# Kernel optimization log

Hardware: AMD Instinct MI355X
Metric: run time of the kernel (lower is better)

The kernel has to match this reference:

```python
import jax, jax.numpy as jnp
import numpy as np

N_TOK, BATCH, D, MEM, H, W = 196, 64, 256, 2048, 16, 16


def setup_inputs() -> dict:
    key = jax.random.key(0)
    ks = jax.random.split(key, 9)
    w_scale = 1.0 / np.sqrt(D)  # ~ Linear default init scale
    return {
        "input_tokens": jax.random.normal(ks[0], (N_TOK, BATCH, D), jnp.float32),
        "ch_memory": jax.random.normal(ks[1], (MEM, D), jnp.float32) * 0.1,
        "ch_wq": jax.random.normal(ks[2], (D, D), jnp.float32) * w_scale,
        "ch_wk": jax.random.normal(ks[3], (D, D), jnp.float32) * w_scale,
        "ch_wv": jax.random.normal(ks[4], (D, D), jnp.float32) * w_scale,
        "sp_memory": jax.random.normal(ks[5], (MEM, H, W), jnp.float32) * 0.1,
        "sp_wq": jax.random.normal(ks[6], (D, D), jnp.float32) * w_scale,
        "sp_wk": jax.random.normal(ks[7], (D, D), jnp.float32) * w_scale,
        "sp_wv": jax.random.normal(ks[8], (D, D), jnp.float32) * w_scale,
    }


def reference(input_tokens, ch_memory, ch_wq, ch_wk, ch_wv,
              sp_memory, sp_wq, sp_wk, sp_wv):
    n_tok, batch, d = input_tokens.shape
    hw = d  # spatial branch requires feature_dim == H*W
    x = input_tokens.reshape(n_tok * batch, d)  # [NB, D]

    # ---- Channel memory branch: dot-product softmax read ----
    q = x @ ch_wq.T                       # [NB, D]
    k = ch_memory @ ch_wk.T               # [M, D]
    v = ch_memory @ ch_wv.T               # [M, D]
    scores = (q @ k.T) * (1.0 / jnp.sqrt(jnp.float32(d)))  # [NB, M]
    att_c = jax.nn.softmax(scores, axis=-1)
    out_c = att_c @ v                     # [NB, D]

    # ---- Spatial memory branch: SSIM-score softmax read ----
    mem_flat = sp_memory.reshape(sp_memory.shape[0], hw)  # [M, HW]
    qf = x @ sp_wq.T                      # [NB, HW]
    kf = mem_flat @ sp_wk.T               # [M, HW]
    vf = mem_flat @ sp_wv.T               # [M, HW]

    q_mean = jnp.mean(qf, axis=1, keepdims=True)          # [NB, 1]
    k_mean = jnp.mean(kf, axis=1, keepdims=True)          # [M, 1]
    q_var = jnp.var(qf, axis=1, ddof=1, keepdims=True)    # unbiased, like torch.var
    k_var = jnp.var(kf, axis=1, ddof=1, keepdims=True)
    cov = ((qf - q_mean) @ (kf - k_mean).T) / jnp.float32(hw - 1)  # [NB, M]

    c1, c2 = 0.01, 0.03
    mean_prod = q_mean @ k_mean.T                          # [NB, M]
    numerator = (2.0 * mean_prod + c1) * (2.0 * cov + c2)
    denominator = (q_mean ** 2 + (k_mean.T) ** 2 + c1) * (q_var + k_var.T + c2)
    ssim = numerator / (denominator + 1e-8)                # [NB, M]

    att_s = jax.nn.softmax(ssim, axis=-1)
    out_s = att_s @ vf                     # [NB, HW] == [NB, D]

    return (out_c + out_s).reshape(n_tok, batch, d)
```

## Files before the change

### kernel.cpp

```cpp
#include <hip/hip_runtime.h>

#define NBQ 12544
#define DM  256
#define MM  2048

typedef __attribute__((ext_vector_type(8)))  __bf16 bf16x8;
typedef __attribute__((ext_vector_type(4)))  float  floatx4;

__device__ __forceinline__ ushort f2bf(float x) {
    unsigned u = __float_as_uint(x);
    u += 0x7fffu + ((u >> 16) & 1u);
    return (ushort)(u >> 16);
}
__device__ __forceinline__ float bf2f(ushort h) {
    return __uint_as_float(((unsigned)h) << 16);
}
__device__ __forceinline__ ushort4 cvt4(float4 f) {
    union { __bf16 h[4]; ushort4 u; } r;
    r.h[0] = (__bf16)f.x; r.h[1] = (__bf16)f.y;
    r.h[2] = (__bf16)f.z; r.h[3] = (__bf16)f.w;
    return r.u;
}

__device__ __forceinline__ void glds16(const ushort* g, ushort* l) {
    __builtin_amdgcn_global_load_lds(
        (const __attribute__((address_space(1))) unsigned int*)g,
        (__attribute__((address_space(3))) unsigned int*)l, 16, 0, 0);
}

#define WAITVM(N) asm volatile("s_waitcnt vmcnt(" #N ")" ::: "memory")
#define WAITLGKM0 asm volatile("s_waitcnt lgkmcnt(0)" ::: "memory")

__global__ __launch_bounds__(256) void gemm_proj_all(
    const float* __restrict__ x,      const float* __restrict__ ch_mem,
    const float* __restrict__ ch_wq,  const float* __restrict__ ch_wk,
    const float* __restrict__ ch_wv,  const float* __restrict__ sp_mem,
    const float* __restrict__ sp_wq,  const float* __restrict__ sp_wk,
    const float* __restrict__ sp_wv,
    ushort* __restrict__ Qb,  ushort* __restrict__ QFb,
    ushort* __restrict__ Kb,  ushort* __restrict__ KFb,
    ushort* __restrict__ Vtb, ushort* __restrict__ VFtb)
{
    __shared__ ushort As[64][72];
    __shared__ ushort W1s[64][72];
    __shared__ ushort W2s[64][72];

    int bid = blockIdx.x;
    const float* A; const float* W1; const float* W2;
    ushort* C1; ushort* C2; int nrows, trans2;
    if (bid < 784) {
        A = x; W1 = ch_wq; W2 = sp_wq; C1 = Qb; C2 = QFb; nrows = NBQ; trans2 = 0;
    } else if (bid < 912) {
        A = ch_mem; W1 = ch_wk; W2 = ch_wv; C1 = Kb; C2 = Vtb;
        nrows = MM; trans2 = 1; bid -= 784;
    } else {
        A = sp_mem; W1 = sp_wk; W2 = sp_wv; C1 = KFb; C2 = VFtb;
        nrows = MM; trans2 = 1; bid -= 912;
    }
    const int r0 = (bid >> 2) * 64;
    const int c0 = (bid & 3) * 64;

    const int tid  = threadIdx.x;
    const int wv   = tid >> 6;
    const int lane = tid & 63;
    const int quad = lane >> 4;
    const int l16  = lane & 15;
    const int rw = (wv & 1) * 32;
    const int cw = (wv >> 1) * 32;

    floatx4 acc1[2][2], acc2[2][2];
    #pragma unroll
    for (int i = 0; i < 2; ++i)
        #pragma unroll
        for (int j = 0; j < 2; ++j) {
            acc1[i][j] = (floatx4){0.f, 0.f, 0.f, 0.f};
            acc2[i][j] = (floatx4){0.f, 0.f, 0.f, 0.f};
        }

    float4 a4[4], w14[4], w24[4];
    #pragma unroll
    for (int it = 0; it < 4; ++it) {
        int idx = tid + it * 256;
        int r = idx >> 4, c4 = (idx & 15) * 4;
        a4[it]  = *(const float4*)(A  + (size_t)(r0 + r) * 256 + c4);
        w14[it] = *(const float4*)(W1 + (size_t)(c0 + r) * 256 + c4);
        w24[it] = *(const float4*)(W2 + (size_t)(c0 + r) * 256 + c4);
    }

    for (int d0 = 0; d0 < 256; d0 += 64) {
        __syncthreads();
        #pragma unroll
        for (int it = 0; it < 4; ++it) {
            int idx = tid + it * 256;
            int r = idx >> 4, c4 = (idx & 15) * 4;
            *(ushort4*)&As[r][c4]  = cvt4(a4[it]);
            *(ushort4*)&W1s[r][c4] = cvt4(w14[it]);
            *(ushort4*)&W2s[r][c4] = cvt4(w24[it]);
        }
        if (d0 + 64 < 256) {
            #pragma unroll
            for (int it = 0; it < 4; ++it) {
                int idx = tid + it * 256;
                int r = idx >> 4, c4 = (idx & 15) * 4;
                a4[it]  = *(const float4*)(A  + (size_t)(r0 + r) * 256 + d0 + 64 + c4);
                w14[it] = *(const float4*)(W1 + (size_t)(c0 + r) * 256 + d0 + 64 + c4);
                w24[it] = *(const float4*)(W2 + (size_t)(c0 + r) * 256 + d0 + 64 + c4);
            }
        }
        __syncthreads();
        #pragma unroll
        for (int kk = 0; kk < 64; kk += 32) {
            bf16x8 aA0 = *(const bf16x8*)&As[rw + l16][kk + quad * 8];
            bf16x8 aA1 = *(const bf16x8*)&As[rw + 16 + l16][kk + quad * 8];
            bf16x8 b10 = *(const bf16x8*)&W1s[cw + l16][kk + quad * 8];
            bf16x8 b11 = *(const bf16x8*)&W1s[cw + 16 + l16][kk + quad * 8];
            bf16x8 b20 = *(const bf16x8*)&W2s[cw + l16][kk + quad * 8];
            bf16x8 b21 = *(const bf16x8*)&W2s[cw + 16 + l16][kk + quad * 8];
            acc1[0][0] = __builtin_amdgcn_mfma_f32_16x16x32_bf16(aA0, b10, acc1[0][0], 0, 0, 0);
            acc1[0][1] = __builtin_amdgcn_mfma_f32_16x16x32_bf16(aA0, b11, acc1[0][1], 0, 0, 0);
            acc1[1][0] = __builtin_amdgcn_mfma_f32_16x16x32_bf16(aA1, b10, acc1[1][0], 0, 0, 0);
            acc1[1][1] = __builtin_amdgcn_mfma_f32_16x16x32_bf16(aA1, b11, acc1[1][1], 0, 0, 0);
            acc2[0][0] = __builtin_amdgcn_mfma_f32_16x16x32_bf16(aA0, b20, acc2[0][0], 0, 0, 0);
            acc2[0][1] = __builtin_amdgcn_mfma_f32_16x16x32_bf16(aA0, b21, acc2[0][1], 0, 0, 0);
            acc2[1][0] = __builtin_amdgcn_mfma_f32_16x16x32_bf16(aA1, b20, acc2[1][0], 0, 0, 0);
            acc2[1][1] = __builtin_amdgcn_mfma_f32_16x16x32_bf16(aA1, b21, acc2[1][1], 0, 0, 0);
        }
    }

    #pragma unroll
    for (int ag = 0; ag < 2; ++ag)
        #pragma unroll
        for (int cg = 0; cg < 2; ++cg)
            #pragma unroll
            for (int i = 0; i < 4; ++i)
                C1[(size_t)(r0 + rw + ag * 16 + quad * 4 + i) * 256
                   + c0 + cw + cg * 16 + l16] = f2bf(acc1[ag][cg][i]);

    if (!trans2) {
        #pragma unroll
        for (int ag = 0; ag < 2; ++ag)
            #pragma unroll
            for (int cg = 0; cg < 2; ++cg)
                #pragma unroll
                for (int i = 0; i < 4; ++i)
                    C2[(size_t)(r0 + rw + ag * 16 + quad * 4 + i) * 256
                       + c0 + cw + cg * 16 + l16] = f2bf(acc2[ag][cg][i]);
    } else {
        __syncthreads();
        #pragma unroll
        for (int ag = 0; ag < 2; ++ag)
            #pragma unroll
            for (int cg = 0; cg < 2; ++cg)
                #pragma unroll
                for (int i = 0; i < 4; ++i)
                    W2s[cw + cg * 16 + l16][rw + ag * 16 + quad * 4 + i] = f2bf(acc2[ag][cg][i]);
        __syncthreads();
        const int col = tid >> 2;
        const int seg = (tid & 3) * 16;
        #pragma unroll
        for (int j = 0; j < 2; ++j)
            *(uint4*)(C2 + (size_t)(c0 + col) * nrows + r0 + seg + j * 8) =
                *(const uint4*)&W2s[col][seg + j * 8];
    }
}

__global__ __launch_bounds__(256) void row_stats_kf(
    const ushort* __restrict__ KFb, float* __restrict__ km, float* __restrict__ kv)
{
    const int row  = blockIdx.x * 4 + (threadIdx.x >> 6);
    const int lane = threadIdx.x & 63;
    ushort4 u = *(const ushort4*)(KFb + (size_t)row * 256 + lane * 4);
    float a = bf2f(u.x), b = bf2f(u.y), c = bf2f(u.z), d = bf2f(u.w);
    float s  = a + b + c + d;
    float ss = a * a + b * b + c * c + d * d;
    #pragma unroll
    for (int off = 32; off > 0; off >>= 1) {
        s  += __shfl_down(s, off);
        ss += __shfl_down(ss, off);
    }
    if (lane == 0) {
        float m = s * (1.f / 256.f);
        km[row] = m;
        kv[row] = (ss - 256.f * m * m) * (1.f / 255.f) + 0.03f;
    }
}

#define STAGE_TILE(b, ti)                                                     \
    {                                                                         \
        const ushort* kp_ = kp0 + (size_t)(ti) * 32 * DM;                     \
        const ushort* vp_ = vp0 + (ti) * 32;                                  \
        ushort* dst_ = SMu + (b) * 16384;                                     \
        _Pragma("unroll")                                                     \
        for (int p = 0; p < 4; ++p) {                                         \
            int db = (wv * 4 + p) * 512;                                      \
            glds16(kp_ + offK[p], dst_ + db);                                 \
            glds16(vp_ + offV[p], dst_ + 8192 + db);                          \
        }                                                                     \
    }

__global__ __launch_bounds__(256, 2) void fused_attn_x4(
    const ushort* __restrict__ Qb,  const ushort* __restrict__ QFb,
    const ushort* __restrict__ Kb,  const ushort* __restrict__ KFb,
    const ushort* __restrict__ Vtb, const ushort* __restrict__ VFtb,
    const float* __restrict__ km_, const float* __restrict__ kv_,
    float* __restrict__ part, float* __restrict__ denp)
{
    __shared__ ushort SMu[32768];

    const int tid  = threadIdx.x;
    const int wv   = tid >> 6;
    const int lane = tid & 63;
    const int quad = lane >> 4;
    const int l16  = lane & 15;

    const int k8   = blockIdx.x & 7;
    const int j    = blockIdx.x >> 3;
    const int br   = (j >= 49) ? 1 : 0;
    const int half = k8 & 3;
    const int qc   = (k8 >> 2) * 49 + (br ? j - 49 : j);
    const int q0   = qc * 128;
    const int kbase = half * 512;
    const int NT   = 16;

    const ushort* qsrc = br ? QFb : Qb;
    const ushort* Ksel = br ? KFb : Kb;
    const ushort* Vsel = br ? VFtb : Vtb;

    bf16x8 aQ0[8], aQ1[8];
    {
        const ushort* qp = qsrc + (size_t)(q0 + wv * 32 + l16) * DM + quad * 8;
        #pragma unroll
        for (int s = 0; s < 8; ++s) {
            aQ0[s] = __builtin_nontemporal_load((const bf16x8*)(qp + s * 32));
            aQ1[s] = __builtin_nontemporal_load((const bf16x8*)(qp + 16 * DM + s * 32));
        }
    }

    float qmv0 = 0.f, qvv0 = 0.f, qmv1 = 0.f, qvv1 = 0.f, qm2_0 = 0.f, qm2_1 = 0.f;
    if (br) {
        float s0 = 0.f, ss0 = 0.f, s1 = 0.f, ss1 = 0.f;
        #pragma unroll
        for (int s = 0; s < 8; ++s)
            #pragma unroll
            for (int jj = 0; jj < 8; ++jj) {
                float v0 = (float)aQ0[s][jj], v1 = (float)aQ1[s][jj];
                s0 += v0; ss0 += v0 * v0; s1 += v1; ss1 += v1 * v1;
            }
        s0  += __shfl_xor(s0, 16, 64);  s0  += __shfl_xor(s0, 32, 64);
        ss0 += __shfl_xor(ss0, 16, 64); ss0 += __shfl_xor(ss0, 32, 64);
        s1  += __shfl_xor(s1, 16, 64);  s1  += __shfl_xor(s1, 32, 64);
        ss1 += __shfl_xor(ss1, 16, 64); ss1 += __shfl_xor(ss1, 32, 64);
        qmv0 = s0 * (1.f / 256.f);
        qvv0 = (ss0 - 256.f * qmv0 * qmv0) * (1.f / 255.f);
        qmv1 = s1 * (1.f / 256.f);
        qvv1 = (ss1 - 256.f * qmv1 * qmv1) * (1.f / 255.f);
        qm2_0 = qmv0 * qmv0 + 0.01f;
        qm2_1 = qmv1 * qmv1 + 0.01f;
    }

    int offK[4], offV[4];
    #pragma unroll
    for (int p = 0; p < 4; ++p) {
        int jw = wv * 4 + p;
        int Rk = 2 * jw + (lane >> 5);
        int rk = (Rk & 3) + ((Rk >> 4) & 1) * 4 + ((Rk >> 2) & 3) * 8;
        int ck = (lane & 31) ^ (Rk & 7);
        offK[p] = rk * DM + ck * 8;
        int Rv = 16 * jw + (lane >> 2);
        int cv = (lane & 3) ^ (Rv & 3);
        offV[p] = Rv * MM + cv * 8;
    }

    const ushort* kp0 = Ksel + (size_t)kbase * DM;
    const ushort* vp0 = Vsel + kbase;

    floatx4 acc0[16], acc1[16];
    #pragma unroll
    for (int t = 0; t < 16; ++t) {
        acc0[t] = (floatx4){0.f, 0.f, 0.f, 0.f};
        acc1[t] = (floatx4){0.f, 0.f, 0.f, 0.f};
    }
    float den0 = 0.f, den1 = 0.f;
    const int ksw  = l16 & 7;
    const int vswo = (quad ^ (l16 & 3)) * 8;

    floatx4 kmc0 = {0,0,0,0}, kmc1 = {0,0,0,0}, kvc0 = {0,0,0,0}, kvc1 = {0,0,0,0};

    STAGE_TILE(0, 0);
    if (br) {
        kmc0 = *(const floatx4*)(km_ + kbase + 8 * quad);
        kmc1 = *(const floatx4*)(km_ + kbase + 8 * quad + 4);
        kvc0 = *(const floatx4*)(kv_ + kbase + 8 * quad);
        kvc1 = *(const floatx4*)(kv_ + kbase + 8 * quad + 4);
    }

    int buf = 0;
    for (int ti = 0; ti < NT; ++ti) {
        const bool have_next = (ti + 1 < NT);
        floatx4 kmn0 = {0,0,0,0}, kmn1 = {0,0,0,0}, kvn0 = {0,0,0,0}, kvn1 = {0,0,0,0};
        if (have_next) {
            STAGE_TILE(buf ^ 1, ti + 1);
            if (br) {
                const int kk1 = kbase + (ti + 1) * 32;
                kmn0 = *(const floatx4*)(km_ + kk1 + 8 * quad);
                kmn1 = *(const floatx4*)(km_ + kk1 + 8 * quad + 4);
                kvn0 = *(const floatx4*)(kv_ + kk1 + 8 * quad);
                kvn1 = *(const floatx4*)(kv_ + kk1 + 8 * quad + 4);
            }
        }
        if (have_next) { if (br) WAITVM(12); else WAITVM(8); }
        else           { WAITVM(0); }
        __builtin_amdgcn_sched_barrier(0);
        __builtin_amdgcn_s_barrier();
        __builtin_amdgcn_sched_barrier(0);

        const ushort* Ks = SMu + buf * 16384;
        const ushort* Vs = Ks + 8192;

        floatx4 S00 = (floatx4){0.f, 0.f, 0.f, 0.f};
        floatx4 S10 = (floatx4){0.f, 0.f, 0.f, 0.f};
        floatx4 S01 = (floatx4){0.f, 0.f, 0.f, 0.f};
        floatx4 S11 = (floatx4){0.f, 0.f, 0.f, 0.f};
        #pragma unroll
        for (int s = 0; s < 8; ++s) {
            int off = ((s * 4 + quad) ^ ksw) * 8;
            bf16x8 aK0 = *(const bf16x8*)(Ks + l16 * DM + off);
            bf16x8 aK1 = *(const bf16x8*)(Ks + 4096 + l16 * DM + off);
            S00 = __builtin_amdgcn_mfma_f32_16x16x32_bf16(aK0, aQ0[s], S00, 0, 0, 0);
            S10 = __builtin_amdgcn_mfma_f32_16x16x32_bf16(aK1, aQ0[s], S10, 0, 0, 0);
            S01 = __builtin_amdgcn_mfma_f32_16x16x32_bf16(aK0, aQ1[s], S01, 0, 0, 0);
            S11 = __builtin_amdgcn_mfma_f32_16x16x32_bf16(aK1, aQ1[s], S11, 0, 0, 0);
        }

        float p0[8], p1[8];
        if (!br) {
            #pragma unroll
            for (int r = 0; r < 4; ++r) {
                p0[r]     = __expf(S00[r] * 0.0625f);
                p0[4 + r] = __expf(S10[r] * 0.0625f);
                p1[r]     = __expf(S01[r] * 0.0625f);
                p1[4 + r] = __expf(S11[r] * 0.0625f);
            }
        } else {
            #pragma unroll
            for (int r = 0; r < 4; ++r) {
                {
                    float kmr = kmc0[r];
                    float mp  = qmv0 * kmr;
                    float cov = (S00[r] - 256.f * mp) * (1.f / 255.f);
                    float num = (2.f * mp + 0.01f) * (2.f * cov + 0.03f);
                    float dn  = (qm2_0 + kmr * kmr) * (qvv0 + kvc0[r]) + 1e-8f;
                    p0[r] = __expf(num / dn);
                }
                {
                    float kmr = kmc1[r];
                    float mp  = qmv0 * kmr;
                    float cov = (S10[r] - 256.f * mp) * (1.f / 255.f);
                    float num = (2.f * mp + 0.01f) * (2.f * cov + 0.03f);
                    float dn  = (qm2_0 + kmr * kmr) * (qvv0 + kvc1[r]) + 1e-8f;
                    p0[4 + r] = __expf(num / dn);
                }
                {
                    float kmr = kmc0[r];
                    float mp  = qmv1 * kmr;
                    float cov = (S01[r] - 256.f * mp) * (1.f / 255.f);
                    float num = (2.f * mp + 0.01f) * (2.f * cov + 0.03f);
                    float dn  = (qm2_1 + kmr * kmr) * (qvv1 + kvc0[r]) + 1e-8f;
                    p1[r] = __expf(num / dn);
                }
                {
                    float kmr = kmc1[r];
                    float mp  = qmv1 * kmr;
                    float cov = (S11[r] - 256.f * mp) * (1.f / 255.f);
                    float num = (2.f * mp + 0.01f) * (2.f * cov + 0.03f);
                    float dn  = (qm2_1 + kmr * kmr) * (qvv1 + kvc1[r]) + 1e-8f;
                    p1[4 + r] = __expf(num / dn);
                }
            }
        }
        union { __bf16 h[8]; bf16x8 v; } ap0, ap1;
        #pragma unroll
        for (int jj = 0; jj < 8; ++jj) {
            den0 += p0[jj]; ap0.h[jj] = (__bf16)p0[jj];
            den1 += p1[jj]; ap1.h[jj] = (__bf16)p1[jj];
        }

        #pragma unroll
        for (int t = 0; t < 16; ++t) {
            bf16x8 bV = *(const bf16x8*)(Vs + (t * 16 + l16) * 32 + vswo);
            acc0[t] = __builtin_amdgcn_mfma_f32_16x16x32_bf16(ap0.v, bV, acc0[t], 0, 0, 0);
            acc1[t] = __builtin_amdgcn_mfma_f32_16x16x32_bf16(ap1.v, bV, acc1[t], 0, 0, 0);
        }

        WAITLGKM0;
        __builtin_amdgcn_sched_barrier(0);
        __builtin_amdgcn_s_barrier();
        __builtin_amdgcn_sched_barrier(0);

        kmc0 = kmn0; kmc1 = kmn1; kvc0 = kvn0; kvc1 = kvn1;
        buf ^= 1;
    }

    den0 += __shfl_xor(den0, 16, 64); den0 += __shfl_xor(den0, 32, 64);
    den1 += __shfl_xor(den1, 16, 64); den1 += __shfl_xor(den1, 32, 64);

    const int sec = br * 4 + half;
    float* Np = part + (size_t)sec * ((size_t)NBQ * DM);
    #pragma unroll
    for (int t = 0; t < 16; ++t)
        #pragma unroll
        for (int r = 0; r < 4; ++r) {
            int row = q0 + wv * 32 + quad * 4 + r;
            __builtin_nontemporal_store(acc0[t][r], &Np[(size_t)row * DM + t * 16 + l16]);
            __builtin_nontemporal_store(acc1[t][r], &Np[(size_t)(row + 16) * DM + t * 16 + l16]);
        }
    if (lane < 16) {
        denp[(size_t)sec * NBQ + q0 + wv * 32 + lane]      = den0;
        denp[(size_t)sec * NBQ + q0 + wv * 32 + 16 + lane] = den1;
    }
}

__global__ __launch_bounds__(256, 2) void fused_attn_fb(
    const ushort* __restrict__ Qb,  const ushort* __restrict__ QFb,
    const ushort* __restrict__ Kb,  const ushort* __restrict__ KFb,
    const ushort* __restrict__ Vtb, const ushort* __restrict__ VFtb,
    const float* __restrict__ km_, const float* __restrict__ kv_,
    float* __restrict__ out)
{
    __shared__ ushort SMu[32768];
    float* combuf = (float*)SMu;

    const int tid  = threadIdx.x;
    const int wv   = tid >> 6;
    const int lane = tid & 63;
    const int quad = lane >> 4;
    const int l16  = lane & 15;
    const int qsel = wv & 1;
    const int br   = wv >> 1;
    const int q0   = blockIdx.x * 32;

    const ushort* qsrc = br ? QFb : Qb;
    bf16x8 aQ[8];
    {
        const ushort* qp = qsrc + (size_t)(q0 + qsel * 16 + l16) * DM + quad * 8;
        #pragma unroll
        for (int s = 0; s < 8; ++s) aQ[s] = *(const bf16x8*)(qp + s * 32);
    }

    float qmv = 0.f, qvv = 0.f, qm2 = 0.f;
    if (br) {
        float sum = 0.f, ss = 0.f;
        #pragma unroll
        for (int s = 0; s < 8; ++s)
            #pragma unroll
            for (int jj = 0; jj < 8; ++jj) {
                float v = (float)aQ[s][jj];
                sum += v; ss += v * v;
            }
        sum += __shfl_xor(sum, 16, 64); sum += __shfl_xor(sum, 32, 64);
        ss  += __shfl_xor(ss, 16, 64);  ss  += __shfl_xor(ss, 32, 64);
        qmv = sum * (1.f / 256.f);
        qvv = (ss - 256.f * qmv * qmv) * (1.f / 255.f);
        qm2 = qmv * qmv + 0.01f;
    }

    int offK[4], offV[4];
    #pragma unroll
    for (int p = 0; p < 4; ++p) {
        int jw = wv * 4 + p;
        int Rk = 2 * jw + (lane >> 5);
        int rk = (Rk & 3) + ((Rk >> 4) & 1) * 4 + ((Rk >> 2) & 3) * 8;
        int ck = (lane & 31) ^ (Rk & 7);
        offK[p] = rk * DM + ck * 8;
        int Rv = 16 * jw + (lane >> 2);
        int cv = (lane & 3) ^ (Rv & 3);
        offV[p] = Rv * MM + cv * 8;
    }

    const ushort* kp  = Kb;
    const ushort* kfp = KFb;
    const ushort* vp  = Vtb;
    const ushort* vfp = VFtb;

    floatx4 acc[16];
    #pragma unroll
    for (int t = 0; t < 16; ++t) acc[t] = (floatx4){0.f, 0.f, 0.f, 0.f};
    float den = 0.f;

    const int ksw  = l16 & 7;
    const int vswo = (quad ^ (l16 & 3)) * 8;

    for (int kt = 0; kt < MM; kt += 32) {
        __syncthreads();
        #pragma unroll
        for (int p = 0; p < 4; ++p) {
            int db = (wv * 4 + p) * 512;
            glds16(kp  + offK[p], SMu + db);
            glds16(kfp + offK[p], SMu + 8192 + db);
            glds16(vp  + offV[p], SMu + 16384 + db);
            glds16(vfp + offV[p], SMu + 24576 + db);
        }
        kp += 32 * DM; kfp += 32 * DM; vp += 32; vfp += 32;
        __syncthreads();

        const ushort* Ks = SMu + (br ? 8192 : 0);
        floatx4 S0 = (floatx4){0.f, 0.f, 0.f, 0.f};
        floatx4 S1 = (floatx4){0.f, 0.f, 0.f, 0.f};
        #pragma unroll
        for (int s = 0; s < 8; ++s) {
            int off = ((s * 4 + quad) ^ ksw) * 8;
            bf16x8 aK0 = *(const bf16x8*)(Ks + l16 * DM + off);
            bf16x8 aK1 = *(const bf16x8*)(Ks + 4096 + l16 * DM + off);
            S0 = __builtin_amdgcn_mfma_f32_16x16x32_bf16(aK0, aQ[s], S0, 0, 0, 0);
            S1 = __builtin_amdgcn_mfma_f32_16x16x32_bf16(aK1, aQ[s], S1, 0, 0, 0);
        }

        float pb[8];
        if (!br) {
            #pragma unroll
            for (int r = 0; r < 4; ++r) {
                pb[r]     = __expf(S0[r] * 0.0625f);
                pb[4 + r] = __expf(S1[r] * 0.0625f);
            }
        } else {
            floatx4 km0 = *(const floatx4*)(km_ + kt + 8 * quad);
            floatx4 km1 = *(const floatx4*)(km_ + kt + 8 * quad + 4);
            floatx4 kv0 = *(const floatx4*)(kv_ + kt + 8 * quad);
            floatx4 kv1 = *(const floatx4*)(kv_ + kt + 8 * quad + 4);
            #pragma unroll
            for (int r = 0; r < 4; ++r) {
                {
                    float kmr = km0[r];
                    float mp  = qmv * kmr;
                    float cov = (S0[r] - 256.f * mp) * (1.f / 255.f);
                    float num = (2.f * mp + 0.01f) * (2.f * cov + 0.03f);
                    float dn  = (qm2 + kmr * kmr) * (qvv + kv0[r]) + 1e-8f;
                    pb[r] = __expf(num / dn);
                }
                {
                    float kmr = km1[r];
                    float mp  = qmv * kmr;
                    float cov = (S1[r] - 256.f * mp) * (1.f / 255.f);
                    float num = (2.f * mp + 0.01f) * (2.f * cov + 0.03f);
                    float dn  = (qm2 + kmr * kmr) * (qvv + kv1[r]) + 1e-8f;
                    pb[4 + r] = __expf(num / dn);
                }
            }
        }
        union { __bf16 h[8]; bf16x8 v; } ap;
        #pragma unroll
        for (int jj = 0; jj < 8; ++jj) {
            den += pb[jj];
            ap.h[jj] = (__bf16)pb[jj];
        }

        const ushort* Vs = SMu + (br ? 24576 : 16384);
        #pragma unroll
        for (int t = 0; t < 16; ++t) {
            bf16x8 bV = *(const bf16x8*)(Vs + (t * 16 + l16) * 32 + vswo);
            acc[t] = __builtin_amdgcn_mfma_f32_16x16x32_bf16(ap.v, bV, acc[t], 0, 0, 0);
        }
    }

    den += __shfl_xor(den, 16, 64);
    den += __shfl_xor(den, 32, 64);
    float rdn[4];
    #pragma unroll
    for (int r = 0; r < 4; ++r)
        rdn[r] = 1.f / __shfl(den, quad * 4 + r, 64);

    __syncthreads();
    if (br) {
        #pragma unroll
        for (int t = 0; t < 16; ++t)
            #pragma unroll
            for (int r = 0; r < 4; ++r)
                combuf[(qsel * 16 + quad * 4 + r) * 256 + t * 16 + l16] = acc[t][r] * rdn[r];
    }
    __syncthreads();
    if (!br) {
        #pragma unroll
        for (int t = 0; t < 16; ++t)
            #pragma unroll
            for (int r = 0; r < 4; ++r) {
                int ql = qsel * 16 + quad * 4 + r;
                out[(size_t)(q0 + ql) * DM + t * 16 + l16] =
                    acc[t][r] * rdn[r] + combuf[ql * 256 + t * 16 + l16];
            }
    }
}

__global__ __launch_bounds__(256) void combine_halves(
    const float* __restrict__ part, const float* __restrict__ denp,
    float* __restrict__ out)
{
    const size_t stride = (size_t)NBQ * 64;
    const floatx4* p4 = (const floatx4*)part;
    floatx4* o4 = (floatx4*)out;
    #pragma unroll
    for (int u = 0; u < 2; ++u) {
        size_t i = (size_t)blockIdx.x * 512 + (size_t)u * 256 + threadIdx.x;
        int q = (int)(i >> 6);
        float dc = 0.f, ds = 0.f;
        #pragma unroll
        for (int h = 0; h < 4; ++h) {
            dc += denp[(size_t)h * NBQ + q];
            ds += denp[(size_t)(4 + h) * NBQ + q];
        }
        float rc = 1.f / dc, rs = 1.f / ds;
        floatx4 nc = {0.f, 0.f, 0.f, 0.f}, ns = {0.f, 0.f, 0.f, 0.f};
        #pragma unroll
        for (int h = 0; h < 4; ++h) {
            floatx4 c = __builtin_nontemporal_load(&p4[(size_t)h * stride + i]);
            floatx4 s = __builtin_nontemporal_load(&p4[(size_t)(4 + h) * stride + i]);
            nc += c;
            ns += s;
        }
        o4[i] = nc * rc + ns * rs;
    }
}

extern "C" void kernel_launch(void* const* d_in, const int* in_sizes, int n_in,
                              void* d_out, int out_size, void* d_ws, size_t ws_size,
                              hipStream_t stream)
{
    const float* x      = (const float*)d_in[0];
    const float* ch_mem = (const float*)d_in[1];
    const float* ch_wq  = (const float*)d_in[2];
    const float* ch_wk  = (const float*)d_in[3];
    const float* ch_wv  = (const float*)d_in[4];
    const float* sp_mem = (const float*)d_in[5];
    const float* sp_wq  = (const float*)d_in[6];
    const float* sp_wk  = (const float*)d_in[7];
    const float* sp_wv  = (const float*)d_in[8];
    float* out = (float*)d_out;

    ushort* Qb   = (ushort*)d_ws;
    ushort* QFb  = Qb   + (size_t)NBQ * DM;
    ushort* Kb   = QFb  + (size_t)NBQ * DM;
    ushort* KFb  = Kb   + (size_t)MM * DM;
    ushort* Vtb  = KFb  + (size_t)MM * DM;
    ushort* VFtb = Vtb  + (size_t)MM * DM;
    float*  km   = (float*)(VFtb + (size_t)MM * DM);
    float*  kv   = km + MM;
    float*  denp = kv + MM;
    float*  part = denp + (size_t)8 * NBQ;

    const size_t base_b = (size_t)((char*)part - (char*)d_ws);
    const size_t need4  = base_b + (size_t)8 * NBQ * DM * sizeof(float);

    dim3 blk(256);
    gemm_proj_all<<<dim3(1040), blk, 0, stream>>>(
        x, ch_mem, ch_wq, ch_wk, ch_wv, sp_mem, sp_wq, sp_wk, sp_wv,
        Qb, QFb, Kb, KFb, Vtb, VFtb);
    row_stats_kf<<<dim3(MM / 4), blk, 0, stream>>>(KFb, km, kv);
    if (ws_size >= need4) {
        fused_attn_x4<<<dim3(784), blk, 0, stream>>>(
            Qb, QFb, Kb, KFb, Vtb, VFtb, km, kv, part, denp);
        combine_halves<<<dim3(NBQ * DM / 4 / 512), blk, 0, stream>>>(part, denp, out);
    } else {
        fused_attn_fb<<<dim3(NBQ / 32), blk, 0, stream>>>(
            Qb, QFb, Kb, KFb, Vtb, VFtb, km, kv, out);
    }
}
```

Before: 306.7 us.

## Split attention block into eight waves of 16 query rows each

The fused attention kernel now uses 512-thread blocks where each of eight waves handles 16 query rows instead of 32, which halves per-wave accumulator registers and cooperative staging work. The hand-tuned vmcnt waits, sched barriers and prefetched km/kv registers are replaced by plain __syncthreads and in-loop loads. Block-to-work mapping is also reordered so spatial-branch blocks come first. This trades per-wave K/V reuse and finer pipelining control for more resident waves to hide latency.

After: 282.7 us. 1.09x faster.

```diff
diff --git a/kernel.cpp b/kernel.cpp
--- a/kernel.cpp
+++ b/kernel.cpp
@@ -27,9 +27,6 @@
         (const __attribute__((address_space(1))) unsigned int*)g,
         (__attribute__((address_space(3))) unsigned int*)l, 16, 0, 0);
 }
-
-#define WAITVM(N) asm volatile("s_waitcnt vmcnt(" #N ")" ::: "memory")
-#define WAITLGKM0 asm volatile("s_waitcnt lgkmcnt(0)" ::: "memory")
 
 __global__ __launch_bounds__(256) void gemm_proj_all(
     const float* __restrict__ x,      const float* __restrict__ ch_mem,
@@ -191,14 +188,14 @@
         const ushort* vp_ = vp0 + (ti) * 32;                                  \
         ushort* dst_ = SMu + (b) * 16384;                                     \
         _Pragma("unroll")                                                     \
-        for (int p = 0; p < 4; ++p) {                                         \
-            int db = (wv * 4 + p) * 512;                                      \
+        for (int p = 0; p < 2; ++p) {                                         \
+            int db = (wv * 2 + p) * 512;                                      \
             glds16(kp_ + offK[p], dst_ + db);                                 \
             glds16(vp_ + offV[p], dst_ + 8192 + db);                          \
         }                                                                     \
     }
 
-__global__ __launch_bounds__(256, 2) void fused_attn_x4(
+__global__ __launch_bounds__(512, 4) void fused_attn_8w(
     const ushort* __restrict__ Qb,  const ushort* __restrict__ QFb,
     const ushort* __restrict__ Kb,  const ushort* __restrict__ KFb,
     const ushort* __restrict__ Vtb, const ushort* __restrict__ VFtb,
@@ -213,11 +210,11 @@
     const int quad = lane >> 4;
     const int l16  = lane & 15;
 
-    const int k8   = blockIdx.x & 7;
-    const int j    = blockIdx.x >> 3;
-    const int br   = (j >= 49) ? 1 : 0;
-    const int half = k8 & 3;
-    const int qc   = (k8 >> 2) * 49 + (br ? j - 49 : j);
+    int bid = blockIdx.x;
+    const int br  = (bid < 392) ? 1 : 0;
+    int rem = br ? bid : bid - 392;
+    const int half = rem / 98;
+    const int qc   = rem - half * 98;
     const int q0   = qc * 128;
     const int kbase = half * 512;
     const int NT   = 16;
@@ -226,42 +223,34 @@
     const ushort* Ksel = br ? KFb : Kb;
     const ushort* Vsel = br ? VFtb : Vtb;
 
-    bf16x8 aQ0[8], aQ1[8];
+    bf16x8 aQ[8];
     {
-        const ushort* qp = qsrc + (size_t)(q0 + wv * 32 + l16) * DM + quad * 8;
-        #pragma unroll
-        for (int s = 0; s < 8; ++s) {
-            aQ0[s] = __builtin_nontemporal_load((const bf16x8*)(qp + s * 32));
-            aQ1[s] = __builtin_nontemporal_load((const bf16x8*)(qp + 16 * DM + s * 32));
-        }
-    }
-
-    float qmv0 = 0.f, qvv0 = 0.f, qmv1 = 0.f, qvv1 = 0.f, qm2_0 = 0.f, qm2_1 = 0.f;
+        const ushort* qp = qsrc + (size_t)(q0 + wv * 16 + l16) * DM + quad * 8;
+        #pragma unroll
+        for (int s = 0; s < 8; ++s) aQ[s] = *(const bf16x8*)(qp + s * 32);
+    }
+
+    float qmv = 0.f, qvv = 0.f, qm2 = 0.f;
     if (br) {
-        float s0 = 0.f, ss0 = 0.f, s1 = 0.f, ss1 = 0.f;
+        float sum = 0.f, ss = 0.f;
         #pragma unroll
         for (int s = 0; s < 8; ++s)
             #pragma unroll
             for (int jj = 0; jj < 8; ++jj) {
-                float v0 = (float)aQ0[s][jj], v1 = (float)aQ1[s][jj];
-                s0 += v0; ss0 += v0 * v0; s1 += v1; ss1 += v1 * v1;
-            }
-        s0  += __shfl_xor(s0, 16, 64);  s0  += __shfl_xor(s0, 32, 64);
-        ss0 += __shfl_xor(ss0, 16, 64); ss0 += __shfl_xor(ss0, 32, 64);
-        s1  += __shfl_xor(s1, 16, 64);  s1  += __shfl_xor(s1, 32, 64);
-        ss1 += __shfl_xor(ss1, 16, 64); ss1 += __shfl_xor(ss1, 32, 64);
-        qmv0 = s0 * (1.f / 256.f);
-        qvv0 = (ss0 - 256.f * qmv0 * qmv0) * (1.f / 255.f);
-        qmv1 = s1 * (1.f / 256.f);
-        qvv1 = (ss1 - 256.f * qmv1 * qmv1) * (1.f / 255.f);
-        qm2_0 = qmv0 * qmv0 + 0.01f;
-        qm2_1 = qmv1 * qmv1 + 0.01f;
-    }
-
-    int offK[4], offV[4];
-    #pragma unroll
-    for (int p = 0; p < 4; ++p) {
-        int jw = wv * 4 + p;
+                float v = (float)aQ[s][jj];
+                sum += v; ss += v * v;
+            }
+        sum += __shfl_xor(sum, 16, 64); sum += __shfl_xor(sum, 32, 64);
+        ss  += __shfl_xor(ss, 16, 64);  ss  += __shfl_xor(ss, 32, 64);
+        qmv = sum * (1.f / 256.f);
+        qvv = (ss - 256.f * qmv * qmv) * (1.f / 255.f);
+        qm2 = qmv * qmv + 0.01f;
+    }
+
+    int offK[2], offV[2];
+    #pragma unroll
+    for (int p = 0; p < 2; ++p) {
+        int jw = wv * 2 + p;
         int Rk = 2 * jw + (lane >> 5);
         int rk = (Rk & 3) + ((Rk >> 4) & 1) * 4 + ((Rk >> 2) & 3) * 8;
         int ck = (lane & 31) ^ (Rk & 7);
@@ -274,236 +263,23 @@
     const ushort* kp0 = Ksel + (size_t)kbase * DM;
     const ushort* vp0 = Vsel + kbase;
 
-    floatx4 acc0[16], acc1[16];
-    #pragma unroll
-    for (int t = 0; t < 16; ++t) {
-        acc0[t] = (floatx4){0.f, 0.f, 0.f, 0.f};
-        acc1[t] = (floatx4){0.f, 0.f, 0.f, 0.f};
-    }
-    float den0 = 0.f, den1 = 0.f;
+    floatx4 acc[16];
+    #pragma unroll
+    for (int t = 0; t < 16; ++t) acc[t] = (floatx4){0.f, 0.f, 0.f, 0.f};
+    float den = 0.f;
     const int ksw  = l16 & 7;
     const int vswo = (quad ^ (l16 & 3)) * 8;
 
-    floatx4 kmc0 = {0,0,0,0}, kmc1 = {0,0,0,0}, kvc0 = {0,0,0,0}, kvc1 = {0,0,0,0};
-
     STAGE_TILE(0, 0);
-    if (br) {
-        kmc0 = *(const floatx4*)(km_ + kbase + 8 * quad);
-        kmc1 = *(const floatx4*)(km_ + kbase + 8 * quad + 4);
-        kvc0 = *(const floatx4*)(kv_ + kbase + 8 * quad);
-        kvc1 = *(const floatx4*)(kv_ + kbase + 8 * quad + 4);
-    }
+    __syncthreads();
 
     int buf = 0;
     for (int ti = 0; ti < NT; ++ti) {
-        const bool have_next = (ti + 1 < NT);
-        floatx4 kmn0 = {0,0,0,0}, kmn1 = {0,0,0,0}, kvn0 = {0,0,0,0}, kvn1 = {0,0,0,0};
-        if (have_next) {
-            STAGE_TILE(buf ^ 1, ti + 1);
-            if (br) {
-                const int kk1 = kbase + (ti + 1) * 32;
-                kmn0 = *(const floatx4*)(km_ + kk1 + 8 * quad);
-                kmn1 = *(const floatx4*)(km_ + kk1 + 8 * quad + 4);
-                kvn0 = *(const floatx4*)(kv_ + kk1 + 8 * quad);
-                kvn1 = *(const floatx4*)(kv_ + kk1 + 8 * quad + 4);
-            }
-        }
-        if (have_next) { if (br) WAITVM(12); else WAITVM(8); }
-        else           { WAITVM(0); }
-        __builtin_amdgcn_sched_barrier(0);
-        __builtin_amdgcn_s_barrier();
-        __builtin_amdgcn_sched_barrier(0);
+        if (ti + 1 < NT) STAGE_TILE(buf ^ 1, ti + 1);
 
         const ushort* Ks = SMu + buf * 16384;
         const ushort* Vs = Ks + 8192;
 
-        floatx4 S00 = (floatx4){0.f, 0.f, 0.f, 0.f};
-        floatx4 S10 = (floatx4){0.f, 0.f, 0.f, 0.f};
-        floatx4 S01 = (floatx4){0.f, 0.f, 0.f, 0.f};
-        floatx4 S11 = (floatx4){0.f, 0.f, 0.f, 0.f};
-        #pragma unroll
-        for (int s = 0; s < 8; ++s) {
-            int off = ((s * 4 + quad) ^ ksw) * 8;
-            bf16x8 aK0 = *(const bf16x8*)(Ks + l16 * DM + off);
-            bf16x8 aK1 = *(const bf16x8*)(Ks + 4096 + l16 * DM + off);
-            S00 = __builtin_amdgcn_mfma_f32_16x16x32_bf16(aK0, aQ0[s], S00, 0, 0, 0);
-            S10 = __builtin_amdgcn_mfma_f32_16x16x32_bf16(aK1, aQ0[s], S10, 0, 0, 0);
-            S01 = __builtin_amdgcn_mfma_f32_16x16x32_bf16(aK0, aQ1[s], S01, 0, 0, 0);
-            S11 = __builtin_amdgcn_mfma_f32_16x16x32_bf16(aK1, aQ1[s], S11, 0, 0, 0);
-        }
-
-        float p0[8], p1[8];
-        if (!br) {
-            #pragma unroll
-            for (int r = 0; r < 4; ++r) {
-                p0[r]     = __expf(S00[r] * 0.0625f);
-                p0[4 + r] = __expf(S10[r] * 0.0625f);
-                p1[r]     = __expf(S01[r] * 0.0625f);
-                p1[4 + r] = __expf(S11[r] * 0.0625f);
-            }
-        } else {
-            #pragma unroll
-            for (int r = 0; r < 4; ++r) {
-                {
-                    float kmr = kmc0[r];
-                    float mp  = qmv0 * kmr;
-                    float cov = (S00[r] - 256.f * mp) * (1.f / 255.f);
-                    float num = (2.f * mp + 0.01f) * (2.f * cov + 0.03f);
-                    float dn  = (qm2_0 + kmr * kmr) * (qvv0 + kvc0[r]) + 1e-8f;
-                    p0[r] = __expf(num / dn);
-                }
-                {
-                    float kmr = kmc1[r];
-                    float mp  = qmv0 * kmr;
-                    float cov = (S10[r] - 256.f * mp) * (1.f / 255.f);
-                    float num = (2.f * mp + 0.01f) * (2.f * cov + 0.03f);
-                    float dn  = (qm2_0 + kmr * kmr) * (qvv0 + kvc1[r]) + 1e-8f;
-                    p0[4 + r] = __expf(num / dn);
-                }
-                {
-                    float kmr = kmc0[r];
-                    float mp  = qmv1 * kmr;
-                    float cov = (S01[r] - 256.f * mp) * (1.f / 255.f);
-                    float num = (2.f * mp + 0.01f) * (2.f * cov + 0.03f);
-                    float dn  = (qm2_1 + kmr * kmr) * (qvv1 + kvc0[r]) + 1e-8f;
-                    p1[r] = __expf(num / dn);
-                }
-                {
-                    float kmr = kmc1[r];
-                    float mp  = qmv1 * kmr;
-                    float cov = (S11[r] - 256.f * mp) * (1.f / 255.f);
-                    float num = (2.f * mp + 0.01f) * (2.f * cov + 0.03f);
-                    float dn  = (qm2_1 + kmr * kmr) * (qvv1 + kvc1[r]) + 1e-8f;
-                    p1[4 + r] = __expf(num / dn);
-                }
-            }
-        }
-        union { __bf16 h[8]; bf16x8 v; } ap0, ap1;
-        #pragma unroll
-        for (int jj = 0; jj < 8; ++jj) {
-            den0 += p0[jj]; ap0.h[jj] = (__bf16)p0[jj];
-            den1 += p1[jj]; ap1.h[jj] = (__bf16)p1[jj];
-        }
-
-        #pragma unroll
-        for (int t = 0; t < 16; ++t) {
-            bf16x8 bV = *(const bf16x8*)(Vs + (t * 16 + l16) * 32 + vswo);
-            acc0[t] = __builtin_amdgcn_mfma_f32_16x16x32_bf16(ap0.v, bV, acc0[t], 0, 0, 0);
-            acc1[t] = __builtin_amdgcn_mfma_f32_16x16x32_bf16(ap1.v, bV, acc1[t], 0, 0, 0);
-        }
-
-        WAITLGKM0;
-        __builtin_amdgcn_sched_barrier(0);
-        __builtin_amdgcn_s_barrier();
-        __builtin_amdgcn_sched_barrier(0);
-
-        kmc0 = kmn0; kmc1 = kmn1; kvc0 = kvn0; kvc1 = kvn1;
-        buf ^= 1;
-    }
-
-    den0 += __shfl_xor(den0, 16, 64); den0 += __shfl_xor(den0, 32, 64);
-    den1 += __shfl_xor(den1, 16, 64); den1 += __shfl_xor(den1, 32, 64);
-
-    const int sec = br * 4 + half;
-    float* Np = part + (size_t)sec * ((size_t)NBQ * DM);
-    #pragma unroll
-    for (int t = 0; t < 16; ++t)
-        #pragma unroll
-        for (int r = 0; r < 4; ++r) {
-            int row = q0 + wv * 32 + quad * 4 + r;
-            __builtin_nontemporal_store(acc0[t][r], &Np[(size_t)row * DM + t * 16 + l16]);
-            __builtin_nontemporal_store(acc1[t][r], &Np[(size_t)(row + 16) * DM + t * 16 + l16]);
-        }
-    if (lane < 16) {
-        denp[(size_t)sec * NBQ + q0 + wv * 32 + lane]      = den0;
-        denp[(size_t)sec * NBQ + q0 + wv * 32 + 16 + lane] = den1;
-    }
-}
-
-__global__ __launch_bounds__(256, 2) void fused_attn_fb(
-    const ushort* __restrict__ Qb,  const ushort* __restrict__ QFb,
-    const ushort* __restrict__ Kb,  const ushort* __restrict__ KFb,
-    const ushort* __restrict__ Vtb, const ushort* __restrict__ VFtb,
-    const float* __restrict__ km_, const float* __restrict__ kv_,
-    float* __restrict__ out)
-{
-    __shared__ ushort SMu[32768];
-    float* combuf = (float*)SMu;
-
-    const int tid  = threadIdx.x;
-    const int wv   = tid >> 6;
-    const int lane = tid & 63;
-    const int quad = lane >> 4;
-    const int l16  = lane & 15;
-    const int qsel = wv & 1;
-    const int br   = wv >> 1;
-    const int q0   = blockIdx.x * 32;
-
-    const ushort* qsrc = br ? QFb : Qb;
-    bf16x8 aQ[8];
-    {
-        const ushort* qp = qsrc + (size_t)(q0 + qsel * 16 + l16) * DM + quad * 8;
-        #pragma unroll
-        for (int s = 0; s < 8; ++s) aQ[s] = *(const bf16x8*)(qp + s * 32);
-    }
-
-    float qmv = 0.f, qvv = 0.f, qm2 = 0.f;
-    if (br) {
-        float sum = 0.f, ss = 0.f;
-        #pragma unroll
-        for (int s = 0; s < 8; ++s)
-            #pragma unroll
-            for (int jj = 0; jj < 8; ++jj) {
-                float v = (float)aQ[s][jj];
-                sum += v; ss += v * v;
-            }
-        sum += __shfl_xor(sum, 16, 64); sum += __shfl_xor(sum, 32, 64);
-        ss  += __shfl_xor(ss, 16, 64);  ss  += __shfl_xor(ss, 32, 64);
-        qmv = sum * (1.f / 256.f);
-        qvv = (ss - 256.f * qmv * qmv) * (1.f / 255.f);
-        qm2 = qmv * qmv + 0.01f;
-    }
-
-    int offK[4], offV[4];
-    #pragma unroll
-    for (int p = 0; p < 4; ++p) {
-        int jw = wv * 4 + p;
-        int Rk = 2 * jw + (lane >> 5);
-        int rk = (Rk & 3) + ((Rk >> 4) & 1) * 4 + ((Rk >> 2) & 3) * 8;
-        int ck = (lane & 31) ^ (Rk & 7);
-        offK[p] = rk * DM + ck * 8;
-        int Rv = 16 * jw + (lane >> 2);
-        int cv = (lane & 3) ^ (Rv & 3);
-        offV[p] = Rv * MM + cv * 8;
-    }
-
-    const ushort* kp  = Kb;
-    const ushort* kfp = KFb;
-    const ushort* vp  = Vtb;
-    const ushort* vfp = VFtb;
-
-    floatx4 acc[16];
-    #pragma unroll
-    for (int t = 0; t < 16; ++t) acc[t] = (floatx4){0.f, 0.f, 0.f, 0.f};
-    float den = 0.f;
-
-    const int ksw  = l16 & 7;
-    const int vswo = (quad ^ (l16 & 3)) * 8;
-
-    for (int kt = 0; kt < MM; kt += 32) {
-        __syncthreads();
-        #pragma unroll
-        for (int p = 0; p < 4; ++p) {
-            int db = (wv * 4 + p) * 512;
-            glds16(kp  + offK[p], SMu + db);
-            glds16(kfp + offK[p], SMu + 8192 + db);
-            glds16(vp  + offV[p], SMu + 16384 + db);
-            glds16(vfp + offV[p], SMu + 24576 + db);
-        }
-        kp += 32 * DM; kfp += 32 * DM; vp += 32; vfp += 32;
-        __syncthreads();
-
-        const ushort* Ks = SMu + (br ? 8192 : 0);
         floatx4 S0 = (floatx4){0.f, 0.f, 0.f, 0.f};
         floatx4 S1 = (floatx4){0.f, 0.f, 0.f, 0.f};
         #pragma unroll
@@ -515,6 +291,7 @@
             S1 = __builtin_amdgcn_mfma_f32_16x16x32_bf16(aK1, aQ[s], S1, 0, 0, 0);
         }
 
+        const int kk = kbase + ti * 32;
         float pb[8];
         if (!br) {
             #pragma unroll
@@ -523,10 +300,10 @@
                 pb[4 + r] = __expf(S1[r] * 0.0625f);
             }
         } else {
-            floatx4 km0 = *(const floatx4*)(km_ + kt + 8 * quad);
-            floatx4 km1 = *(const floatx4*)(km_ + kt + 8 * quad + 4);
-            floatx4 kv0 = *(const floatx4*)(kv_ + kt + 8 * quad);
-            floatx4 kv1 = *(const floatx4*)(kv_ + kt + 8 * quad + 4);
+            floatx4 km0 = *(const floatx4*)(km_ + kk + 8 * quad);
+            floatx4 km1 = *(const floatx4*)(km_ + kk + 8 * quad + 4);
+            floatx4 kv0 = *(const floatx4*)(kv_ + kk + 8 * quad);
+            floatx4 kv1 = *(const floatx4*)(kv_ + kk + 8 * quad + 4);
             #pragma unroll
             for (int r = 0; r < 4; ++r) {
                 {
@@ -554,6 +331,166 @@
             ap.h[jj] = (__bf16)pb[jj];
         }
 
+        #pragma unroll
+        for (int t = 0; t < 16; ++t) {
+            bf16x8 bV = *(const bf16x8*)(Vs + (t * 16 + l16) * 32 + vswo);
+            acc[t] = __builtin_amdgcn_mfma_f32_16x16x32_bf16(ap.v, bV, acc[t], 0, 0, 0);
+        }
+
+        __syncthreads();
+        buf ^= 1;
+    }
+
+    den += __shfl_xor(den, 16, 64);
+    den += __shfl_xor(den, 32, 64);
+
+    const int sec = br * 4 + half;
+    float* Np = part + (size_t)sec * ((size_t)NBQ * DM);
+    #pragma unroll
+    for (int t = 0; t < 16; ++t)
+        #pragma unroll
+        for (int r = 0; r < 4; ++r) {
+            int row = q0 + wv * 16 + quad * 4 + r;
+            Np[(size_t)row * DM + t * 16 + l16] = acc[t][r];
+        }
+    if (lane < 16)
+        denp[(size_t)sec * NBQ + q0 + wv * 16 + lane] = den;
+}
+
+__global__ __launch_bounds__(256, 2) void fused_attn_fb(
+    const ushort* __restrict__ Qb,  const ushort* __restrict__ QFb,
+    const ushort* __restrict__ Kb,  const ushort* __restrict__ KFb,
+    const ushort* __restrict__ Vtb, const ushort* __restrict__ VFtb,
+    const float* __restrict__ km_, const float* __restrict__ kv_,
+    float* __restrict__ out)
+{
+    __shared__ ushort SMu[32768];
+    float* combuf = (float*)SMu;
+
+    const int tid  = threadIdx.x;
+    const int wv   = tid >> 6;
+    const int lane = tid & 63;
+    const int quad = lane >> 4;
+    const int l16  = lane & 15;
+    const int qsel = wv & 1;
+    const int br   = wv >> 1;
+    const int q0   = blockIdx.x * 32;
+
+    const ushort* qsrc = br ? QFb : Qb;
+    bf16x8 aQ[8];
+    {
+        const ushort* qp = qsrc + (size_t)(q0 + qsel * 16 + l16) * DM + quad * 8;
+        #pragma unroll
+        for (int s = 0; s < 8; ++s) aQ[s] = *(const bf16x8*)(qp + s * 32);
+    }
+
+    float qmv = 0.f, qvv = 0.f, qm2 = 0.f;
+    if (br) {
+        float sum = 0.f, ss = 0.f;
+        #pragma unroll
+        for (int s = 0; s < 8; ++s)
+            #pragma unroll
+            for (int jj = 0; jj < 8; ++jj) {
+                float v = (float)aQ[s][jj];
+                sum += v; ss += v * v;
+            }
+        sum += __shfl_xor(sum, 16, 64); sum += __shfl_xor(sum, 32, 64);
+        ss  += __shfl_xor(ss, 16, 64);  ss  += __shfl_xor(ss, 32, 64);
+        qmv = sum * (1.f / 256.f);
+        qvv = (ss - 256.f * qmv * qmv) * (1.f / 255.f);
+        qm2 = qmv * qmv + 0.01f;
+    }
+
+    int offK[4], offV[4];
+    #pragma unroll
+    for (int p = 0; p < 4; ++p) {
+        int jw = wv * 4 + p;
+        int Rk = 2 * jw + (lane >> 5);
+        int rk = (Rk & 3) + ((Rk >> 4) & 1) * 4 + ((Rk >> 2) & 3) * 8;
+        int ck = (lane & 31) ^ (Rk & 7);
+        offK[p] = rk * DM + ck * 8;
+        int Rv = 16 * jw + (lane >> 2);
+        int cv = (lane & 3) ^ (Rv & 3);
+        offV[p] = Rv * MM + cv * 8;
+    }
+
+    const ushort* kp  = Kb;
+    const ushort* kfp = KFb;
+    const ushort* vp  = Vtb;
+    const ushort* vfp = VFtb;
+
+    floatx4 acc[16];
+    #pragma unroll
+    for (int t = 0; t < 16; ++t) acc[t] = (floatx4){0.f, 0.f, 0.f, 0.f};
+    float den = 0.f;
+
+    const int ksw  = l16 & 7;
+    const int vswo = (quad ^ (l16 & 3)) * 8;
+
+    for (int kt = 0; kt < MM; kt += 32) {
+        __syncthreads();
+        #pragma unroll
+        for (int p = 0; p < 4; ++p) {
+            int db = (wv * 4 + p) * 512;
+            glds16(kp  + offK[p], SMu + db);
+            glds16(kfp + offK[p], SMu + 8192 + db);
+            glds16(vp  + offV[p], SMu + 16384 + db);
+            glds16(vfp + offV[p], SMu + 24576 + db);
+        }
+        kp += 32 * DM; kfp += 32 * DM; vp += 32; vfp += 32;
+        __syncthreads();
+
+        const ushort* Ks = SMu + (br ? 8192 : 0);
+        floatx4 S0 = (floatx4){0.f, 0.f, 0.f, 0.f};
+        floatx4 S1 = (floatx4){0.f, 0.f, 0.f, 0.f};
+        #pragma unroll
+        for (int s = 0; s < 8; ++s) {
+            int off = ((s * 4 + quad) ^ ksw) * 8;
+            bf16x8 aK0 = *(const bf16x8*)(Ks + l16 * DM + off);
+            bf16x8 aK1 = *(const bf16x8*)(Ks + 4096 + l16 * DM + off);
+            S0 = __builtin_amdgcn_mfma_f32_16x16x32_bf16(aK0, aQ[s], S0, 0, 0, 0);
+            S1 = __builtin_amdgcn_mfma_f32_16x16x32_bf16(aK1, aQ[s], S1, 0, 0, 0);
+        }
+
+        float pb[8];
+        if (!br) {
+            #pragma unroll
+            for (int r = 0; r < 4; ++r) {
+                pb[r]     = __expf(S0[r] * 0.0625f);
+                pb[4 + r] = __expf(S1[r] * 0.0625f);
+            }
+        } else {
+            floatx4 km0 = *(const floatx4*)(km_ + kt + 8 * quad);
+            floatx4 km1 = *(const floatx4*)(km_ + kt + 8 * quad + 4);
+            floatx4 kv0 = *(const floatx4*)(kv_ + kt + 8 * quad);
+            floatx4 kv1 = *(const floatx4*)(kv_ + kt + 8 * quad + 4);
+            #pragma unroll
+            for (int r = 0; r < 4; ++r) {
+                {
+                    float kmr = km0[r];
+                    float mp  = qmv * kmr;
+                    float cov = (S0[r] - 256.f * mp) * (1.f / 255.f);
+                    float num = (2.f * mp + 0.01f) * (2.f * cov + 0.03f);
+                    float dn  = (qm2 + kmr * kmr) * (qvv + kv0[r]) + 1e-8f;
+                    pb[r] = __expf(num / dn);
+                }
+                {
+                    float kmr = km1[r];
+                    float mp  = qmv * kmr;
+                    float cov = (S1[r] - 256.f * mp) * (1.f / 255.f);
+                    float num = (2.f * mp + 0.01f) * (2.f * cov + 0.03f);
+                    float dn  = (qm2 + kmr * kmr) * (qvv + kv1[r]) + 1e-8f;
+                    pb[4 + r] = __expf(num / dn);
+                }
+            }
+        }
+        union { __bf16 h[8]; bf16x8 v; } ap;
+        #pragma unroll
+        for (int jj = 0; jj < 8; ++jj) {
+            den += pb[jj];
+            ap.h[jj] = (__bf16)pb[jj];
+        }
+
         const ushort* Vs = SMu + (br ? 24576 : 16384);
         #pragma unroll
         for (int t = 0; t < 16; ++t) {
@@ -655,7 +592,7 @@
         Qb, QFb, Kb, KFb, Vtb, VFtb);
     row_stats_kf<<<dim3(MM / 4), blk, 0, stream>>>(KFb, km, kv);
     if (ws_size >= need4) {
-        fused_attn_x4<<<dim3(784), blk, 0, stream>>>(
+        fused_attn_8w<<<dim3(784), dim3(512), 0, stream>>>(
             Qb, QFb, Kb, KFb, Vtb, VFtb, km, kv, part, denp);
         combine_halves<<<dim3(NBQ * DM / 4 / 512), blk, 0, stream>>>(part, denp, out);
     } else {
```
